# Performance work log

Hardware: AMD Instinct MI355X
Metric: run time of the kernel (lower is better)

Reference implementation:

```python
import jax, jax.numpy as jnp
import numpy as np

B, T, H = 2, 2048, 1024
I = 4096            # intermediate dim
HEADS = 4
RET = 128           # private expert retrieval dim
NUM_EXPERTS = 4096
NUM_KEYS = 64       # sqrt(NUM_EXPERTS)
K = 8               # num_cdmmoe_experts_per_head


def setup_inputs() -> dict:
    key = jax.random.key(0)
    ks = jax.random.split(key, 7)
    return {
        "hidden_states": jax.random.normal(ks[0], (B, T, H), jnp.float32),
        "W_up": jax.random.normal(ks[1], (I, H), jnp.float32) * 0.02,
        "W_down": jax.random.normal(ks[2], (H, I), jnp.float32) * 0.02,
        "W_q": jax.random.normal(ks[3], (HEADS * RET, H), jnp.float32) * 0.02,
        "keys": jax.random.normal(ks[4], (HEADS, NUM_KEYS, 2, RET // 2), jnp.float32) * 0.02,
        "down_embed": jax.random.normal(ks[5], (NUM_EXPERTS, H), jnp.float32) * 0.02,
        "up_embed": jax.random.normal(ks[6], (NUM_EXPERTS, H), jnp.float32) * 0.02,
    }


def reference(hidden_states, W_up, W_down, W_q, keys, down_embed, up_embed):
    b, t, hd = hidden_states.shape
    h, nk, _, n = keys.shape  # heads, num_keys, 2, half retrieval dim
    # queries: [b,t,h*2n] -> [2,b,t,h,n]
    q = jnp.einsum('btd,ed->bte', hidden_states, W_q)
    q = q.reshape(b, t, 2, h, n).transpose(2, 0, 1, 3, 4)
    # product-key similarities: [2,b,t,h,num_keys]
    sim = jnp.einsum('pbthn,hkpn->pbthk', q, keys)
    scores_xy, idx_xy = jax.lax.top_k(sim, K)  # [2,b,t,h,K]
    sx, sy = scores_xy[0], scores_xy[1]
    ix, iy = idx_xy[0], idx_xy[1]
    # cartesian combine: [b,t,h,K*K]
    all_scores = (sx[..., :, None] + sy[..., None, :]).reshape(b, t, h, K * K)
    all_idx = (ix[..., :, None] * nk + iy[..., None, :]).reshape(b, t, h, K * K)
    scores, pk = jax.lax.top_k(all_scores, K)               # [b,t,h,K]
    indices = jnp.take_along_axis(all_idx, pk, axis=-1)     # [b,t,h,K]
    de = down_embed[indices]  # [b,t,h,K,H]
    ue = up_embed[indices]    # [b,t,h,K,H]
    w = jax.nn.silu(jnp.einsum('btd,bthkd->bthk', hidden_states, de)
                    * jax.nn.softmax(scores, axis=-1))
    experts_states = jnp.einsum('bthk,bthkd->btd', w, ue)
    dense = jnp.einsum('bti,di->btd', jax.nn.silu(jnp.einsum('btd,id->bti', hidden_states, W_up)), W_down)
    return dense + experts_states
```

## Files before the change

### kernel.cpp

```cpp
#include <hip/hip_runtime.h>

typedef unsigned short u16;
typedef unsigned int u32;

#define TOKENS 4096
#define HDIM 1024
#define IDIM 4096
#define NHEADS 4
#define NKEYS 64
#define TOPK 8
#define QDIM 512

typedef __bf16 bf16x8 __attribute__((ext_vector_type(8)));
typedef float  f32x4  __attribute__((ext_vector_type(4)));
typedef u16    u16x8  __attribute__((ext_vector_type(8)));
typedef u16    u16x4  __attribute__((ext_vector_type(4)));
typedef u32    u32x4  __attribute__((ext_vector_type(4)));

__device__ __forceinline__ u16 f2bf(float f) {
    u32 u = __float_as_uint(f);
    u += 0x7fffu + ((u >> 16) & 1u);
    return (u16)(u >> 16);
}
__device__ __forceinline__ float bf2f(u16 h) { return __uint_as_float(((u32)h) << 16); }

#define H_N4   1048576
#define WUP_N4 1048576
#define WDN_N4 1048576
#define DE_N4  1048576
#define UE_N4  1048576
#define CVT_TOT (H_N4 + WUP_N4 + WDN_N4 + DE_N4 + UE_N4)

__device__ __forceinline__ void cvt1(const float* in, u16* hi, u16* lo, int i) {
    float4 v = reinterpret_cast<const float4*>(in)[i];
    float vf[4] = {v.x, v.y, v.z, v.w};
    ushort4 h;
    u16 hh[4];
#pragma unroll
    for (int j = 0; j < 4; j++) hh[j] = f2bf(vf[j]);
    h.x = hh[0]; h.y = hh[1]; h.z = hh[2]; h.w = hh[3];
    reinterpret_cast<ushort4*>(hi)[i] = h;
    if (lo) {
        ushort4 l4;
        u16 ll[4];
#pragma unroll
        for (int j = 0; j < 4; j++) ll[j] = f2bf(vf[j] - bf2f(hh[j]));
        l4.x = ll[0]; l4.y = ll[1]; l4.z = ll[2]; l4.w = ll[3];
        reinterpret_cast<ushort4*>(lo)[i] = l4;
    }
}

__device__ __forceinline__ void cvt1_f8(const float* in, u32* out8, int i) {
    float4 v = reinterpret_cast<const float4*>(in)[i];
    u32 w = __builtin_amdgcn_cvt_pk_fp8_f32(v.x, v.y, 0u, false);
    w = __builtin_amdgcn_cvt_pk_fp8_f32(v.z, v.w, w, true);
    out8[i] = w;
}

__global__ __launch_bounds__(256) void cvt_all(
    const float* __restrict__ hidden, const float* __restrict__ W_up,
    const float* __restrict__ W_down, const float* __restrict__ de,
    const float* __restrict__ ue,
    u16* __restrict__ hid_hi, u16* __restrict__ hid_lo,
    u16* __restrict__ wup, u16* __restrict__ wdn,
    u32* __restrict__ de_f8, u32* __restrict__ ue_f8) {
    int i = blockIdx.x * 256 + threadIdx.x;
    if (i >= CVT_TOT) return;
    if (i < H_N4) { cvt1(hidden, hid_hi, hid_lo, i); return; }
    i -= H_N4;
    if (i < WUP_N4) { cvt1(W_up, wup, nullptr, i); return; }
    i -= WUP_N4;
    if (i < WDN_N4) { cvt1(W_down, wdn, nullptr, i); return; }
    i -= WDN_N4;
    if (i < DE_N4) { cvt1_f8(de, de_f8, i); return; }
    i -= DE_N4;
    cvt1_f8(ue, ue_f8, i);
}

__global__ __launch_bounds__(256) void weff_kernel(
    const float* __restrict__ keys, const float* __restrict__ Wq,
    u16* __restrict__ weff_hi, u16* __restrict__ weff_lo) {
    __shared__ float kk[64][65];
    __shared__ float wq_s[64][128];

    const int g = blockIdx.x >> 3, ds = blockIdx.x & 7;
    const int p = g >> 2, h = g & 3;
    const int d0 = ds * 128;
    const int t = threadIdx.x;
    const int base = p * 256 + h * 64;

    {
        int k = t >> 2, part = t & 3;
        const float* krow = keys + (((size_t)(h * NKEYS + k) * 2 + p) * 64);
#pragma unroll
        for (int j = 0; j < 4; j++) {
            int n0 = part * 16 + j * 4;
            float4 v = *reinterpret_cast<const float4*>(krow + n0);
            kk[k][n0 + 0] = v.x; kk[k][n0 + 1] = v.y;
            kk[k][n0 + 2] = v.z; kk[k][n0 + 3] = v.w;
        }
    }
    {
        int n = t >> 2, dpart = t & 3;
        const float* wrow = Wq + (size_t)(base + n) * HDIM + d0;
#pragma unroll
        for (int j = 0; j < 8; j++) {
            int dd = dpart * 32 + j * 4;
            float4 v = *reinterpret_cast<const float4*>(wrow + dd);
            *reinterpret_cast<float4*>(&wq_s[n][dd]) = v;
        }
    }
    __syncthreads();

    const int k = t & 63, dq = t >> 6;
    float acc[32];
#pragma unroll
    for (int i = 0; i < 32; i++) acc[i] = 0.f;
    for (int n = 0; n < 64; n++) {
        float kv = kk[k][n];
        const float4* wrow = reinterpret_cast<const float4*>(&wq_s[n][dq * 32]);
#pragma unroll
        for (int j = 0; j < 8; j++) {
            float4 w4 = wrow[j];
            acc[j * 4 + 0] += kv * w4.x; acc[j * 4 + 1] += kv * w4.y;
            acc[j * 4 + 2] += kv * w4.z; acc[j * 4 + 3] += kv * w4.w;
        }
    }
    size_t ro = (size_t)(g * 64 + k) * HDIM + d0 + dq * 32;
#pragma unroll
    for (int j = 0; j < 8; j++) {
        ushort4 hh, ll;
        u16 hv[4], lv[4];
#pragma unroll
        for (int i = 0; i < 4; i++) {
            float a = acc[j * 4 + i];
            hv[i] = f2bf(a);
            lv[i] = f2bf(a - bf2f(hv[i]));
        }
        hh.x = hv[0]; hh.y = hv[1]; hh.z = hv[2]; hh.w = hv[3];
        ll.x = lv[0]; ll.y = lv[1]; ll.z = lv[2]; ll.w = lv[3];
        *reinterpret_cast<ushort4*>(weff_hi + ro + j * 4) = hh;
        *reinterpret_cast<ushort4*>(weff_lo + ro + j * 4) = ll;
    }
}

__global__ __launch_bounds__(256) void reduce_add(float* __restrict__ out,
                                                  const float* __restrict__ p, int n4) {
    int i = blockIdx.x * 256 + threadIdx.x;
    if (i >= n4) return;
    float4 a = reinterpret_cast<const float4*>(out)[i];
    float4 b = reinterpret_cast<const float4*>(p)[i];
    a.x += b.x; a.y += b.y; a.z += b.z; a.w += b.w;
    reinterpret_cast<float4*>(out)[i] = a;
}

__device__ __forceinline__ void gload16(const void* g, void* s) {
    auto gp = reinterpret_cast<const __attribute__((address_space(1))) u32*>(
        reinterpret_cast<uintptr_t>(g));
    auto sp = reinterpret_cast<__attribute__((address_space(3))) u32*>(
        reinterpret_cast<uintptr_t>(s));
    __builtin_amdgcn_global_load_lds(gp, sp, 16, 0, 0);
}

#define BK 32

__device__ __forceinline__ int swz(int a) { return a ^ (((a >> 7) & 3) << 4); }

template <int ROWS>
__device__ __forceinline__ void stage_tile(const u16* g, size_t krow_b, size_t kb0,
                                           u16* s, int t) {
#pragma unroll
    for (int rnd = 0; rnd < ROWS / 64; rnd++) {
        int o = t * 16 + rnd * 4096;
        int os = swz(o);
        int row = o >> 6, kb = os & 63;
        gload16((const char*)g + (size_t)row * krow_b + kb0 + kb, (char*)s + o);
    }
}

template <int EPI, int TBM, int TBN, bool SPLIT, int KCHUNKS>
__global__ __launch_bounds__(256) void gemm_bt(
    const u16* __restrict__ A, const u16* __restrict__ Alo,
    const u16* __restrict__ B, const u16* __restrict__ Blo,
    void* __restrict__ Cout, void* __restrict__ Cout2,
    const float* __restrict__ ext, int M, int N, int K) {
    constexpr int NS = SPLIT ? 2 : 1;
    constexpr int WM = TBM / 2, WN = TBN / 2;
    constexpr int FM = WM / 16, FN = WN / 16;
    constexpr int ASZ = NS * TBM * BK;
    constexpr int BSZ = NS * TBN * BK;
    __shared__ u16 As[2][ASZ];
    __shared__ u16 Bs[2][BSZ];
    const int t = threadIdx.x;
    const int lane = t & 63;
    const int wave = t >> 6;
    const int wr = wave >> 1, wc = wave & 1;
    const int m0 = blockIdx.y * TBM;
    const int n0 = blockIdx.x * TBN;
    const int klen = K / KCHUNKS;
    const int koff = (KCHUNKS > 1) ? blockIdx.z * klen : 0;

    f32x4 acc[FM][FN];
#pragma unroll
    for (int i = 0; i < FM; i++)
#pragma unroll
        for (int j = 0; j < FN; j++) acc[i][j] = (f32x4){0.f, 0.f, 0.f, 0.f};

    const size_t krow = (size_t)K * 2;
    const int ro = lane & 15;
    const int ko = (lane >> 4) * 16;

    const u16* Ab = A + (size_t)m0 * K;
    const u16* Bb = B + (size_t)n0 * K;
    const u16* Alb = SPLIT ? Alo + (size_t)m0 * K : nullptr;
    const u16* Blb = SPLIT ? Blo + (size_t)n0 * K : nullptr;

    auto stage_all = [&](int b, int k0) {
        size_t kb0 = (size_t)k0 * 2;
        stage_tile<TBM>(Ab, krow, kb0, As[b], t);
        stage_tile<TBN>(Bb, krow, kb0, Bs[b], t);
        if (SPLIT) {
            stage_tile<TBM>(Alb, krow, kb0, As[b] + TBM * BK, t);
            stage_tile<TBN>(Blb, krow, kb0, Bs[b] + TBN * BK, t);
        }
    };

    stage_all(0, koff);
    __syncthreads();
    int cur = 0;

    for (int k0 = koff; k0 < koff + klen; k0 += BK) {
        if (k0 + BK < koff + klen) stage_all(cur ^ 1, k0 + BK);
        const u16* Ac = As[cur];
        const u16* Bc = Bs[cur];
        bf16x8 fa[FM], fb[FN], fal[FM], fbl[FN];
#pragma unroll
        for (int i = 0; i < FM; i++) {
            int a = swz((wr * WM + i * 16 + ro) * 64 + ko);
            fa[i] = *reinterpret_cast<const bf16x8*>((const char*)Ac + a);
            if (SPLIT)
                fal[i] = *reinterpret_cast<const bf16x8*>((const char*)(Ac + TBM * BK) + a);
        }
#pragma unroll
        for (int j = 0; j < FN; j++) {
            int a = swz((wc * WN + j * 16 + ro) * 64 + ko);
            fb[j] = *reinterpret_cast<const bf16x8*>((const char*)Bc + a);
            if (SPLIT)
                fbl[j] = *reinterpret_cast<const bf16x8*>((const char*)(Bc + TBN * BK) + a);
        }
#pragma unroll
        for (int i = 0; i < FM; i++)
#pragma unroll
            for (int j = 0; j < FN; j++) {
                acc[i][j] = __builtin_amdgcn_mfma_f32_16x16x32_bf16(fa[i], fb[j],
                                                                    acc[i][j], 0, 0, 0);
                if (SPLIT) {
                    acc[i][j] = __builtin_amdgcn_mfma_f32_16x16x32_bf16(fa[i], fbl[j],
                                                                        acc[i][j], 0, 0, 0);
                    acc[i][j] = __builtin_amdgcn_mfma_f32_16x16x32_bf16(fal[i], fb[j],
                                                                        acc[i][j], 0, 0, 0);
                }
            }
        __syncthreads();
        cur ^= 1;
    }

#pragma unroll
    for (int i = 0; i < FM; i++)
#pragma unroll
        for (int j = 0; j < FN; j++) {
            int col = n0 + wc * WN + j * 16 + (lane & 15);
            int rbase = m0 + wr * WM + i * 16 + (lane >> 4) * 4;
#pragma unroll
            for (int r = 0; r < 4; r++) {
                int row = rbase + r;
                float v = acc[i][j][r];
                size_t off = (size_t)row * N + col;
                if (EPI == 0) {
                    ((float*)Cout)[off] = v;
                } else if (EPI == 1) {
                    float s = v / (1.f + __expf(-v));
                    ((u16*)Cout)[off] = f2bf(s);
                } else {
                    if (KCHUNKS == 1 || blockIdx.z == 0)
                        ((float*)Cout)[off] = v + ext[off];
                    else
                        ((float*)Cout2)[off] = v;
                }
            }
        }
}

__device__ __forceinline__ int rank64(const float* base, float v, int l) {
    const float4* gv = reinterpret_cast<const float4*>(base);
    int rank = 0;
#pragma unroll
    for (int n = 0; n < 16; n++) {
        float4 o = gv[n];
        int b = n * 4;
        rank += (o.x > v) || (o.x == v && (b + 0) < l);
        rank += (o.y > v) || (o.y == v && (b + 1) < l);
        rank += (o.z > v) || (o.z == v && (b + 2) < l);
        rank += (o.w > v) || (o.w == v && (b + 3) < l);
    }
    return rank;
}

__global__ __launch_bounds__(512) void router(
    const float* __restrict__ Simb,
    int* __restrict__ sidx_g, float* __restrict__ gate_g) {
    __shared__ float sims[QDIM];
    __shared__ float topv[8][TOPK];
    __shared__ int topi[8][TOPK];
    __shared__ float pv[NHEADS][64];
    __shared__ float st8[NHEADS][TOPK];
    __shared__ int sid8[NHEADS][TOPK];

    const int tok = blockIdx.x;
    const int tid = threadIdx.x;
    const int w = tid >> 6, l = tid & 63;

    sims[tid] = Simb[(size_t)tok * QDIM + tid];
    __syncthreads();

    {
        float v = sims[w * 64 + l];
        int rank = rank64(sims + w * 64, v, l);
        if (rank < TOPK) { topv[w][rank] = v; topi[w][rank] = l; }
    }
    __syncthreads();

    if (w < NHEADS) {
        pv[w][l] = topv[w][l >> 3] + topv[4 + w][l & 7];
    }
    __syncthreads();

    if (w < NHEADS) {
        float v = pv[w][l];
        int rank = rank64(pv[w], v, l);
        if (rank < TOPK) {
            st8[w][rank] = v;
            sid8[w][rank] = topi[w][l >> 3] * NKEYS + topi[4 + w][l & 7];
        }
    }
    __syncthreads();

    if (tid < NHEADS * TOPK) {
        int h = tid >> 3, r = tid & 7;
        float m0 = st8[h][0];
        float s = 0.f;
#pragma unroll
        for (int i = 0; i < TOPK; i++) s += __expf(st8[h][i] - m0);
        size_t o = ((size_t)tok * NHEADS + h) * TOPK + r;
        sidx_g[o] = sid8[h][r];
        gate_g[o] = __expf(st8[h][r] - m0) / s;
    }
}

__global__ __launch_bounds__(256) void expert_gather(
    const u16* __restrict__ hid_bf, const u32* __restrict__ de_f8,
    const u32* __restrict__ ue_f8, const int* __restrict__ sidx_g,
    const float* __restrict__ gate_g, float* __restrict__ expst) {
    __shared__ float wks[32];
    __shared__ int eids_s[32];

    const int tok = blockIdx.x;
    const int w = threadIdx.x >> 6, l = threadIdx.x & 63;

    {
        u16x8 hv[2];
        const u16* hrow = hid_bf + (size_t)tok * HDIM + l * 16;
        hv[0] = *reinterpret_cast<const u16x8*>(hrow);
        hv[1] = *reinterpret_cast<const u16x8*>(hrow + 8);
        float h16[16];
#pragma unroll
        for (int t2 = 0; t2 < 8; t2++) { h16[t2] = bf2f(hv[0][t2]); h16[8 + t2] = bf2f(hv[1][t2]); }
        int eid[8];
        float gt[8];
#pragma unroll
        for (int j = 0; j < 8; j++) {
            size_t o = (size_t)tok * 32 + w * 8 + j;
            eid[j] = sidx_g[o];
            gt[j] = gate_g[o];
        }
        u32x4 dv[8];
#pragma unroll
        for (int j = 0; j < 8; j++) {
            const u32x4* dr = reinterpret_cast<const u32x4*>(de_f8 + (size_t)eid[j] * 256 + l * 4);
            dv[j] = *dr;
        }
        float dot[8];
#pragma unroll
        for (int j = 0; j < 8; j++) {
            float s = 0.f;
#pragma unroll
            for (int w2 = 0; w2 < 4; w2++) {
                u32 word = dv[j][w2];
                s += h16[w2 * 4 + 0] * __builtin_amdgcn_cvt_f32_fp8(word, 0);
                s += h16[w2 * 4 + 1] * __builtin_amdgcn_cvt_f32_fp8(word, 1);
                s += h16[w2 * 4 + 2] * __builtin_amdgcn_cvt_f32_fp8(word, 2);
                s += h16[w2 * 4 + 3] * __builtin_amdgcn_cvt_f32_fp8(word, 3);
            }
            dot[j] = s;
        }
#pragma unroll
        for (int m = 32; m; m >>= 1)
#pragma unroll
            for (int j = 0; j < 8; j++) dot[j] += __shfl_xor(dot[j], m, 64);
#pragma unroll
        for (int j = 0; j < 8; j++)
            if (l == j) {
                float x = dot[j] * gt[j];
                wks[w * 8 + j] = x / (1.f + __expf(-x));
                eids_s[w * 8 + j] = eid[j];
            }
    }
    __syncthreads();

    {
        float acc0 = 0.f, acc1 = 0.f, acc2 = 0.f, acc3 = 0.f;
        const u32* ubase = ue_f8 + w * 64 + l;
#pragma unroll
        for (int m = 0; m < 32; m++) {
            int e = eids_s[m];
            float wk = wks[m];
            u32 u = ubase[(size_t)e * 256];
            acc0 += wk * __builtin_amdgcn_cvt_f32_fp8(u, 0);
            acc1 += wk * __builtin_amdgcn_cvt_f32_fp8(u, 1);
            acc2 += wk * __builtin_amdgcn_cvt_f32_fp8(u, 2);
            acc3 += wk * __builtin_amdgcn_cvt_f32_fp8(u, 3);
        }
        float4 a4 = make_float4(acc0, acc1, acc2, acc3);
        *reinterpret_cast<float4*>(expst + (size_t)tok * HDIM + w * 256 + l * 4) = a4;
    }
}

extern "C" void kernel_launch(void* const* d_in, const int* in_sizes, int n_in,
                              void* d_out, int out_size, void* d_ws, size_t ws_size,
                              hipStream_t stream) {
    const float* hidden = (const float*)d_in[0];
    const float* W_up = (const float*)d_in[1];
    const float* W_down = (const float*)d_in[2];
    const float* W_q = (const float*)d_in[3];
    const float* keys = (const float*)d_in[4];
    const float* down_embed = (const float*)d_in[5];
    const float* up_embed = (const float*)d_in[6];
    float* out = (float*)d_out;

    char* ws = (char*)d_ws;
    size_t off = 0;
    auto alloc = [&](size_t bytes) {
        void* p = ws + off;
        off += (bytes + 255) & ~(size_t)255;
        return p;
    };
    u16* hid_hi = (u16*)alloc((size_t)TOKENS * HDIM * 2);
    u16* hid_lo = (u16*)alloc((size_t)TOKENS * HDIM * 2);
    float* Simb = (float*)alloc((size_t)TOKENS * QDIM * 4);
    float* partial = (float*)hid_lo;
    u16* weff_hi = (u16*)alloc((size_t)QDIM * HDIM * 2);
    u16* weff_lo = (u16*)alloc((size_t)QDIM * HDIM * 2);
    u16* wup = (u16*)alloc((size_t)IDIM * HDIM * 2);
    u16* wdn = (u16*)alloc((size_t)HDIM * IDIM * 2);
    u16* act = (u16*)alloc((size_t)TOKENS * IDIM * 2);
    u32* de_f8 = (u32*)alloc((size_t)4096 * HDIM);
    u32* ue_f8 = (u32*)alloc((size_t)4096 * HDIM);
    float* expst = (float*)alloc((size_t)TOKENS * HDIM * 4);
    int* sidx_g = (int*)alloc((size_t)TOKENS * 32 * 4);
    float* gate_g = (float*)alloc((size_t)TOKENS * 32 * 4);

    cvt_all<<<(CVT_TOT + 255) / 256, 256, 0, stream>>>(
        hidden, W_up, W_down, down_embed, up_embed,
        hid_hi, hid_lo, wup, wdn, de_f8, ue_f8);
    weff_kernel<<<64, 256, 0, stream>>>(keys, W_q, weff_hi, weff_lo);

    dim3 blk(256);
    gemm_bt<0, 64, 128, true, 1><<<dim3(QDIM / 128, TOKENS / 64), blk, 0, stream>>>(
        hid_hi, hid_lo, weff_hi, weff_lo, Simb, nullptr, nullptr, TOKENS, QDIM, HDIM);

    router<<<TOKENS, 512, 0, stream>>>(Simb, sidx_g, gate_g);
    expert_gather<<<TOKENS, 256, 0, stream>>>(hid_hi, de_f8, ue_f8, sidx_g, gate_g, expst);

    gemm_bt<1, 128, 128, false, 1><<<dim3(IDIM / 128, TOKENS / 128), blk, 0, stream>>>(
        hid_hi, nullptr, wup, nullptr, act, nullptr, nullptr, TOKENS, IDIM, HDIM);
    gemm_bt<2, 128, 64, false, 2><<<dim3(HDIM / 64, TOKENS / 128, 2), blk, 0, stream>>>(
        act, nullptr, wdn, nullptr, out, partial, expst, TOKENS, HDIM, IDIM);
    reduce_add<<<(TOKENS * HDIM / 4 + 255) / 256, 256, 0, stream>>>(out, partial,
                                                                    TOKENS * HDIM / 4);
}
```

Before: 235.9 us.

## Enlarge GEMM tiles, parameterize wave layout, and add XCD-aware block swizzle

Generalizes the bf16 GEMM kernel so the wave grid and thread count are template parameters. The up-projection now uses 256x128 tiles with 8 waves, and the down-projection moves from 128x64 to 128x128 tiles. An optional block-id remap spreads consecutive blocks across the 8 XCDs. The aim is more operand reuse per tile and better L2 locality, at the cost of fewer blocks per grid, more registers and LDS per block, and possible occupancy and tail effects.

```diff
diff --git a/kernel.cpp b/kernel.cpp
--- a/kernel.cpp
+++ b/kernel.cpp
@@ -166,26 +166,27 @@
 
 __device__ __forceinline__ int swz(int a) { return a ^ (((a >> 7) & 3) << 4); }
 
-template <int ROWS>
+template <int ROWS, int THREADS>
 __device__ __forceinline__ void stage_tile(const u16* g, size_t krow_b, size_t kb0,
                                            u16* s, int t) {
 #pragma unroll
-    for (int rnd = 0; rnd < ROWS / 64; rnd++) {
-        int o = t * 16 + rnd * 4096;
+    for (int rnd = 0; rnd < ROWS * 64 / (THREADS * 16); rnd++) {
+        int o = t * 16 + rnd * THREADS * 16;
         int os = swz(o);
         int row = o >> 6, kb = os & 63;
         gload16((const char*)g + (size_t)row * krow_b + kb0 + kb, (char*)s + o);
     }
 }
 
-template <int EPI, int TBM, int TBN, bool SPLIT, int KCHUNKS>
-__global__ __launch_bounds__(256) void gemm_bt(
+template <int EPI, int TBM, int TBN, int WVM, int WVN, bool SPLIT, int KCHUNKS, bool XSWZ>
+__global__ __launch_bounds__(WVM * WVN * 64) void gemm_bt(
     const u16* __restrict__ A, const u16* __restrict__ Alo,
     const u16* __restrict__ B, const u16* __restrict__ Blo,
     void* __restrict__ Cout, void* __restrict__ Cout2,
     const float* __restrict__ ext, int M, int N, int K) {
+    constexpr int THREADS = WVM * WVN * 64;
     constexpr int NS = SPLIT ? 2 : 1;
-    constexpr int WM = TBM / 2, WN = TBN / 2;
+    constexpr int WM = TBM / WVM, WN = TBN / WVN;
     constexpr int FM = WM / 16, FN = WN / 16;
     constexpr int ASZ = NS * TBM * BK;
     constexpr int BSZ = NS * TBN * BK;
@@ -194,9 +195,19 @@
     const int t = threadIdx.x;
     const int lane = t & 63;
     const int wave = t >> 6;
-    const int wr = wave >> 1, wc = wave & 1;
-    const int m0 = blockIdx.y * TBM;
-    const int n0 = blockIdx.x * TBN;
+    const int wr = wave / WVN, wc = wave % WVN;
+
+    int bx = blockIdx.x, by = blockIdx.y;
+    if (XSWZ) {
+        int gx = gridDim.x, gy = gridDim.y;
+        int n = gx * gy;
+        int bid = by * gx + bx;
+        int q = n >> 3;
+        bid = (bid & 7) * q + (bid >> 3);
+        bx = bid % gx; by = bid / gx;
+    }
+    const int m0 = by * TBM;
+    const int n0 = bx * TBN;
     const int klen = K / KCHUNKS;
     const int koff = (KCHUNKS > 1) ? blockIdx.z * klen : 0;
 
@@ -217,11 +228,11 @@
 
     auto stage_all = [&](int b, int k0) {
         size_t kb0 = (size_t)k0 * 2;
-        stage_tile<TBM>(Ab, krow, kb0, As[b], t);
-        stage_tile<TBN>(Bb, krow, kb0, Bs[b], t);
+        stage_tile<TBM, THREADS>(Ab, krow, kb0, As[b], t);
+        stage_tile<TBN, THREADS>(Bb, krow, kb0, Bs[b], t);
         if (SPLIT) {
-            stage_tile<TBM>(Alb, krow, kb0, As[b] + TBM * BK, t);
-            stage_tile<TBN>(Blb, krow, kb0, Bs[b] + TBN * BK, t);
+            stage_tile<TBM, THREADS>(Alb, krow, kb0, As[b] + TBM * BK, t);
+            stage_tile<TBN, THREADS>(Blb, krow, kb0, Bs[b] + TBN * BK, t);
         }
     };
 
@@ -474,16 +485,18 @@
         hid_hi, hid_lo, wup, wdn, de_f8, ue_f8);
     weff_kernel<<<64, 256, 0, stream>>>(keys, W_q, weff_hi, weff_lo);
 
-    dim3 blk(256);
-    gemm_bt<0, 64, 128, true, 1><<<dim3(QDIM / 128, TOKENS / 64), blk, 0, stream>>>(
+    gemm_bt<0, 64, 128, 2, 2, true, 1, false>
+        <<<dim3(QDIM / 128, TOKENS / 64), 256, 0, stream>>>(
         hid_hi, hid_lo, weff_hi, weff_lo, Simb, nullptr, nullptr, TOKENS, QDIM, HDIM);
 
     router<<<TOKENS, 512, 0, stream>>>(Simb, sidx_g, gate_g);
     expert_gather<<<TOKENS, 256, 0, stream>>>(hid_hi, de_f8, ue_f8, sidx_g, gate_g, expst);
 
-    gemm_bt<1, 128, 128, false, 1><<<dim3(IDIM / 128, TOKENS / 128), blk, 0, stream>>>(
+    gemm_bt<1, 256, 128, 4, 2, false, 1, true>
+        <<<dim3(IDIM / 128, TOKENS / 256), 512, 0, stream>>>(
         hid_hi, nullptr, wup, nullptr, act, nullptr, nullptr, TOKENS, IDIM, HDIM);
-    gemm_bt<2, 128, 64, false, 2><<<dim3(HDIM / 64, TOKENS / 128, 2), blk, 0, stream>>>(
+    gemm_bt<2, 128, 128, 2, 2, false, 2, true>
+        <<<dim3(HDIM / 128, TOKENS / 128, 2), 256, 0, stream>>>(
         act, nullptr, wdn, nullptr, out, partial, expst, TOKENS, HDIM, IDIM);
     reduce_add<<<(TOKENS * HDIM / 4 + 255) / 256, 256, 0, stream>>>(out, partial,
                                                                     TOKENS * HDIM / 4);
```

Measured after the change: 222.7 us. 1.06x faster.
